# Optimization experiments

Measured on AMD Instinct MI355X. Metric: run time of the kernel, lower is better.

## Reference

```python
import jax, jax.numpy as jnp
import numpy as np
from jax import lax

BN_EPS = 1e-5
DELTA_FRAC = 0.7


def ternarize(t):
    """Per-row (dim 0) ternarization: delta = 0.7*mean|t_i|, alpha = mean of |t_i| above delta."""
    B = t.shape[0]
    flat = t.reshape(B, -1)                       # [B, n]
    absf = jnp.abs(flat)
    n = flat.shape[1]
    d = DELTA_FRAC * absf.sum(axis=1) / n         # [B]
    mask = absf > d[:, None]                      # strict >, matching torch code
    count = mask.sum(axis=1).astype(flat.dtype)
    alpha = (absf * mask).sum(axis=1) / count     # [B]
    tern = jnp.where(flat > d[:, None], 1.0, 0.0) + jnp.where(flat < -d[:, None], -1.0, 0.0)
    return (tern * alpha[:, None]).reshape(t.shape)


def conv2d(x, w, b):
    out = lax.conv_general_dilated(x, w, window_strides=(1, 1), padding='VALID',
                                   dimension_numbers=('NCHW', 'OIHW', 'NCHW'))
    return out + b[None, :, None, None]


def maxpool2(x):
    return lax.reduce_window(x, -jnp.inf, lax.max, (1, 1, 2, 2), (1, 1, 2, 2), 'VALID')


def batchnorm_eval(x, gamma, beta):
    # eval-mode BN with running_mean=0, running_var=1
    inv = 1.0 / np.sqrt(1.0 + BN_EPS)
    return x * (gamma[None, :, None, None] * inv) + beta[None, :, None, None]


def setup_inputs() -> dict:
    key = jax.random.key(0)
    ks = jax.random.split(key, 12)
    B = 2048
    inp = {
        'x': jax.random.normal(ks[0], (B, 1, 28, 28), dtype=jnp.float32),
        'conv1_w': jax.random.normal(ks[1], (32, 1, 5, 5), dtype=jnp.float32) * 0.1,
        'conv1_b': jax.random.normal(ks[2], (32,), dtype=jnp.float32) * 0.1,
        'bn1_g': jax.random.normal(ks[3], (32,), dtype=jnp.float32) * 0.1 + 1.0,
        'bn1_b': jax.random.normal(ks[4], (32,), dtype=jnp.float32) * 0.1,
        'conv2_w': jax.random.normal(ks[5], (64, 32, 5, 5), dtype=jnp.float32) * 0.05,
        'conv2_b': jax.random.normal(ks[6], (64,), dtype=jnp.float32) * 0.1,
        'bn2_g': jax.random.normal(ks[7], (64,), dtype=jnp.float32) * 0.1 + 1.0,
        'bn2_b': jax.random.normal(ks[8], (64,), dtype=jnp.float32) * 0.1,
        'fc1_w': jax.random.normal(ks[9], (512, 1024), dtype=jnp.float32) * 0.03,
        'fc1_b': jax.random.normal(ks[10], (512,), dtype=jnp.float32) * 0.1,
        'fc2_w': jax.random.normal(ks[11], (10, 512), dtype=jnp.float32) * 0.05,
        'fc2_b': jnp.zeros((10,), dtype=jnp.float32),
    }
    return inp


def reference(x, conv1_w, conv1_b, bn1_g, bn1_b, conv2_w, conv2_b, bn2_g, bn2_b,
              fc1_w, fc1_b, fc2_w, fc2_b):
    h = ternarize(conv2d(x, conv1_w, conv1_b))            # [B,32,24,24]
    h = jax.nn.relu(maxpool2(batchnorm_eval(h, bn1_g, bn1_b)))  # [B,32,12,12]
    h = ternarize(conv2d(h, conv2_w, conv2_b))            # [B,64,8,8]
    h = jax.nn.relu(maxpool2(batchnorm_eval(h, bn2_g, bn2_b)))  # [B,64,4,4]
    h = h.reshape(-1, 1024)
    h = jax.nn.relu(ternarize(h @ fc1_w.T + fc1_b))       # [B,512]
    out = ternarize(h @ fc2_w.T + fc2_b)                  # [B,10]
    return out
```

## Files before the change

kernel.cpp:

```cpp
#include <hip/hip_runtime.h>

#define BATCH 2048

__device__ __forceinline__ float blockReduceSumF(float v, float* red, int tid, int nwaves) {
  #pragma unroll
  for (int off = 32; off > 0; off >>= 1) v += __shfl_xor(v, off);
  __syncthreads();
  if ((tid & 63) == 0) red[tid >> 6] = v;
  __syncthreads();
  if (tid == 0) {
    float s = red[0];
    for (int i = 1; i < nwaves; i++) s += red[i];
    red[31] = s;
  }
  __syncthreads();
  return red[31];
}

__device__ __forceinline__ float2 blockReduceSum2F(float a, float b, float* red, int tid, int nwaves) {
  #pragma unroll
  for (int off = 32; off > 0; off >>= 1) { a += __shfl_xor(a, off); b += __shfl_xor(b, off); }
  __syncthreads();
  if ((tid & 63) == 0) { red[tid >> 6] = a; red[(tid >> 6) + 16] = b; }
  __syncthreads();
  if (tid == 0) {
    float sa = red[0], sb = red[16];
    for (int i = 1; i < nwaves; i++) { sa += red[i]; sb += red[16 + i]; }
    red[30] = sa; red[31] = sb;
  }
  __syncthreads();
  return make_float2(red[30], red[31]);
}

__device__ __forceinline__ float groupReduce4w(float v, float* seg, int tj) {
  #pragma unroll
  for (int off = 32; off > 0; off >>= 1) v += __shfl_xor(v, off);
  __syncthreads();
  if ((tj & 63) == 0) seg[tj >> 6] = v;
  __syncthreads();
  return (seg[0] + seg[1]) + (seg[2] + seg[3]);
}

__global__ void k0_w2t(const float* __restrict__ w2, float* __restrict__ w2t2) {
  int i = blockIdx.x * 256 + threadIdx.x;
  if (i >= 57344) return;
  int cc = i / 1792;
  int r = i - cc * 1792;
  int c2 = r / 28;
  int k = r - c2 * 28;
  w2t2[i] = (k < 25) ? w2[c2 * 800 + cc * 25 + k] : 0.0f;
}

__global__ __launch_bounds__(512, 4) void k1_conv1(
    const float* __restrict__ x, const float* __restrict__ w1, const float* __restrict__ b1,
    signed char* __restrict__ s1full, float* __restrict__ alpha1) {
  __shared__ float xs[784];
  __shared__ float wsm[800];
  __shared__ float red[32];

  const int tid = threadIdx.x;
  const int smp = blockIdx.x;

  for (int j = tid; j < 784; j += 512) xs[j] = x[smp * 784 + j];
  for (int j = tid; j < 800; j += 512) wsm[j] = w1[j];
  __syncthreads();

  const int c = tid >> 4;
  const int g = tid & 15;
  const float bias = b1[c];
  const float* wc = &wsm[c * 25];

  float a[36];
  float asum = 0.0f;
  #pragma unroll
  for (int tt = 0; tt < 3; tt++) {
    const int t = g + (tt << 4);
    const int r = t >> 1;
    const int hx = (t & 1) * 12;
    float acc[12];
    #pragma unroll
    for (int i = 0; i < 12; i++) acc[i] = bias;
    #pragma unroll
    for (int ky = 0; ky < 5; ky++) {
      const float* xp = &xs[(r + ky) * 28 + hx];
      float xrow[16];
      *(float4*)&xrow[0]  = *(const float4*)&xp[0];
      *(float4*)&xrow[4]  = *(const float4*)&xp[4];
      *(float4*)&xrow[8]  = *(const float4*)&xp[8];
      *(float4*)&xrow[12] = *(const float4*)&xp[12];
      #pragma unroll
      for (int kx = 0; kx < 5; kx++) {
        const float w = wc[ky * 5 + kx];
        #pragma unroll
        for (int i = 0; i < 12; i++) acc[i] = fmaf(xrow[i + kx], w, acc[i]);
      }
    }
    #pragma unroll
    for (int i = 0; i < 12; i++) { a[tt * 12 + i] = acc[i]; asum += fabsf(acc[i]); }
  }

  float tot = blockReduceSumF(asum, red, tid, 8);
  float delta = (0.7f * tot) / 18432.0f;

  float msum = 0.0f, mcnt = 0.0f;
  #pragma unroll
  for (int i = 0; i < 36; i++) {
    float fa = fabsf(a[i]);
    if (fa > delta) { msum += fa; mcnt += 1.0f; }
  }
  float2 mm = blockReduceSum2F(msum, mcnt, red, tid, 8);
  if (tid == 0) alpha1[smp] = (mm.y > 0.0f) ? (mm.x / mm.y) : 0.0f;

  signed char* sp = s1full + (size_t)smp * 18432 + c * 576 + g * 12;
  #pragma unroll
  for (int tt = 0; tt < 3; tt++) {
    int s_[12];
    #pragma unroll
    for (int i = 0; i < 12; i++) {
      float v = a[tt * 12 + i];
      s_[i] = (v > delta) ? 1 : ((v < -delta) ? -1 : 0);
    }
    unsigned u0 = (s_[0] & 0xFF) | ((s_[1] & 0xFF) << 8) | ((s_[2] & 0xFF) << 16) |
                  (((unsigned)(s_[3] & 0xFF)) << 24);
    unsigned u1 = (s_[4] & 0xFF) | ((s_[5] & 0xFF) << 8) | ((s_[6] & 0xFF) << 16) |
                  (((unsigned)(s_[7] & 0xFF)) << 24);
    unsigned u2 = (s_[8] & 0xFF) | ((s_[9] & 0xFF) << 8) | ((s_[10] & 0xFF) << 16) |
                  (((unsigned)(s_[11] & 0xFF)) << 24);
    unsigned* wq = (unsigned*)(sp + tt * 192);
    wq[0] = u0; wq[1] = u1; wq[2] = u2;
  }
}

__global__ __launch_bounds__(256, 3) void k2_conv2(
    const signed char* __restrict__ s1full, const float* __restrict__ alpha1,
    const float* __restrict__ w2t2, const float* __restrict__ b2,
    const float* __restrict__ g1, const float* __restrict__ bt1,
    signed char* __restrict__ s2full, float* __restrict__ alpha2) {
  __shared__ float pooled[4608];
  __shared__ float g1l[32], bt1l[32];
  __shared__ float red[32];

  const int tid = threadIdx.x;
  const int smp = blockIdx.x;
  const float BNINV = (float)(1.0 / sqrt(1.0 + 1e-5));

  if (tid < 32) { g1l[tid] = g1[tid] * BNINV; bt1l[tid] = bt1[tid]; }
  __syncthreads();

  const float a1 = alpha1[smp];
  {
    const int ci = tid >> 3;
    const int o8 = tid & 7;
    int r = o8 * 18;
    int py = (o8 * 3) >> 1;
    int px = r - py * 12;
    const signed char* sbase = s1full + (size_t)smp * 18432 + ci * 576;
    float* pout = &pooled[ci * 144];
    const float gg = g1l[ci], bb = bt1l[ci];
    #pragma unroll
    for (int k = 0; k < 18; k++) {
      const signed char* sp = sbase + py * 48 + px * 2;
      char2 t0 = *(const char2*)sp;
      char2 t1 = *(const char2*)(sp + 24);
      float m = -1e30f;
      { float v = ((float)t0.x * a1) * gg + bb; m = (v > m) ? v : m; }
      { float v = ((float)t0.y * a1) * gg + bb; m = (v > m) ? v : m; }
      { float v = ((float)t1.x * a1) * gg + bb; m = (v > m) ? v : m; }
      { float v = ((float)t1.y * a1) * gg + bb; m = (v > m) ? v : m; }
      pout[py * 12 + px] = (m > 0.0f) ? m : 0.0f;
      px++;
      if (px == 12) { px = 0; py++; }
    }
  }
  __syncthreads();

  const int c2 = tid >> 2;
  const int q = tid & 3;
  const int r0 = q << 1;
  const float bias = b2[c2];
  float acc0[8], acc1[8];
  #pragma unroll
  for (int i = 0; i < 8; i++) { acc0[i] = bias; acc1[i] = bias; }

  const float4* wp = ((const float4*)w2t2) + c2 * 7;
  const float* pb = &pooled[r0 * 12];
  #pragma unroll 1
  for (int cc = 0; cc < 32; cc++) {
    const float4 W0 = wp[0], W1 = wp[1], W2 = wp[2], W3 = wp[3],
                 W4 = wp[4], W5 = wp[5], W6 = wp[6];
    const float wk[25] = {W0.x, W0.y, W0.z, W0.w, W1.x, W1.y, W1.z, W1.w,
                          W2.x, W2.y, W2.z, W2.w, W3.x, W3.y, W3.z, W3.w,
                          W4.x, W4.y, W4.z, W4.w, W5.x, W5.y, W5.z, W5.w, W6.x};
    #pragma unroll
    for (int t = 0; t < 6; t++) {
      float row[12];
      *(float4*)&row[0] = *(const float4*)&pb[t * 12];
      *(float4*)&row[4] = *(const float4*)&pb[t * 12 + 4];
      *(float4*)&row[8] = *(const float4*)&pb[t * 12 + 8];
      #pragma unroll
      for (int ky = 0; ky < 5; ky++) {
        const int i = t - ky;
        if (i == 0) {
          #pragma unroll
          for (int kx = 0; kx < 5; kx++) {
            const float w = wk[ky * 5 + kx];
            #pragma unroll
            for (int ox = 0; ox < 8; ox++) acc0[ox] = fmaf(row[ox + kx], w, acc0[ox]);
          }
        } else if (i == 1) {
          #pragma unroll
          for (int kx = 0; kx < 5; kx++) {
            const float w = wk[ky * 5 + kx];
            #pragma unroll
            for (int ox = 0; ox < 8; ox++) acc1[ox] = fmaf(row[ox + kx], w, acc1[ox]);
          }
        }
      }
    }
    wp += 448;
    pb += 144;
  }

  float asum = 0.0f;
  #pragma unroll
  for (int i = 0; i < 8; i++) asum += fabsf(acc0[i]) + fabsf(acc1[i]);
  float tot = blockReduceSumF(asum, red, tid, 4);
  float delta = (0.7f * tot) / 4096.0f;

  float msum = 0.0f, mcnt = 0.0f;
  #pragma unroll
  for (int i = 0; i < 8; i++) {
    float f0 = fabsf(acc0[i]);
    if (f0 > delta) { msum += f0; mcnt += 1.0f; }
    float f1 = fabsf(acc1[i]);
    if (f1 > delta) { msum += f1; mcnt += 1.0f; }
  }
  float2 mm = blockReduceSum2F(msum, mcnt, red, tid, 4);
  if (tid == 0) alpha2[smp] = (mm.y > 0.0f) ? (mm.x / mm.y) : 0.0f;

  int t_[16];
  #pragma unroll
  for (int ox = 0; ox < 8; ox++) {
    float v = acc0[ox];
    t_[ox] = (v > delta) ? 1 : ((v < -delta) ? -1 : 0);
  }
  #pragma unroll
  for (int ox = 0; ox < 8; ox++) {
    float v = acc1[ox];
    t_[8 + ox] = (v > delta) ? 1 : ((v < -delta) ? -1 : 0);
  }
  unsigned u0 = (t_[0] & 0xFF) | ((t_[1] & 0xFF) << 8) | ((t_[2] & 0xFF) << 16) |
                (((unsigned)(t_[3] & 0xFF)) << 24);
  unsigned u1 = (t_[4] & 0xFF) | ((t_[5] & 0xFF) << 8) | ((t_[6] & 0xFF) << 16) |
                (((unsigned)(t_[7] & 0xFF)) << 24);
  unsigned u2 = (t_[8] & 0xFF) | ((t_[9] & 0xFF) << 8) | ((t_[10] & 0xFF) << 16) |
                (((unsigned)(t_[11] & 0xFF)) << 24);
  unsigned u3 = (t_[12] & 0xFF) | ((t_[13] & 0xFF) << 8) | ((t_[14] & 0xFF) << 16) |
                (((unsigned)(t_[15] & 0xFF)) << 24);
  *(uint4*)(s2full + (size_t)smp * 4096 + c2 * 64 + r0 * 8) = make_uint4(u0, u1, u2, u3);
}

__global__ void k0_transpose(const float* __restrict__ w1f, float* __restrict__ w1t) {
  int i = blockIdx.x * 256 + threadIdx.x;
  int k = i >> 9;
  int o = i & 511;
  w1t[i] = w1f[o * 1024 + k];
}

__global__ __launch_bounds__(1024, 4) void k3_fc(
    const signed char* __restrict__ s2full, const float* __restrict__ alpha2,
    const float* __restrict__ w1t, const float* __restrict__ f1b,
    const float* __restrict__ w2f, const float* __restrict__ f2b,
    const float* __restrict__ g2, const float* __restrict__ bt2,
    float* __restrict__ out) {
  __shared__ float S[16384];
  __shared__ float fco[4][512];
  __shared__ float g2l[64], bt2l[64];
  __shared__ float redm[4][4];
  __shared__ float out2[4][10];

  const int tid = threadIdx.x;
  const int blk = blockIdx.x;
  const float BNINV = (float)(1.0 / sqrt(1.0 + 1e-5));

  if (tid < 64) { g2l[tid] = g2[tid] * BNINV; bt2l[tid] = bt2[tid]; }
  __syncthreads();

  float* h4 = S;
  for (int e = tid; e < 4096; e += 1024) {
    int j = e >> 2;
    int s = e & 3;
    int cc = j >> 4;
    int r = j & 15;
    int py = r >> 2;
    int px = r & 3;
    const signed char* sp = s2full + (size_t)(blk * 4 + s) * 4096 + cc * 64 + (py * 2) * 8 + px * 2;
    float a2 = alpha2[blk * 4 + s];
    float m = -1e30f;
    #pragma unroll
    for (int dy = 0; dy < 2; dy++)
      #pragma unroll
      for (int dx = 0; dx < 2; dx++) {
        float v = ((float)sp[dy * 8 + dx] * a2) * g2l[cc] + bt2l[cc];
        m = (v > m) ? v : m;
      }
    h4[j * 4 + s] = (m > 0.0f) ? m : 0.0f;
  }
  __syncthreads();

  const int kp = tid >> 7;
  const int og = tid & 127;
  float a00=0,a01=0,a02=0,a03=0, a10=0,a11=0,a12=0,a13=0;
  float a20=0,a21=0,a22=0,a23=0, a30=0,a31=0,a32=0,a33=0;
  const float4* w4 = (const float4*)w1t;
  const float4* h44 = (const float4*)h4;
  const int kbase = kp << 7;
  for (int kk = 0; kk < 128; kk++) {
    const int k = kbase + kk;
    const float4 wv = w4[(k << 7) + og];
    const float4 hv = h44[k];
    a00 = fmaf(hv.x, wv.x, a00); a01 = fmaf(hv.y, wv.x, a01);
    a02 = fmaf(hv.z, wv.x, a02); a03 = fmaf(hv.w, wv.x, a03);
    a10 = fmaf(hv.x, wv.y, a10); a11 = fmaf(hv.y, wv.y, a11);
    a12 = fmaf(hv.z, wv.y, a12); a13 = fmaf(hv.w, wv.y, a13);
    a20 = fmaf(hv.x, wv.z, a20); a21 = fmaf(hv.y, wv.z, a21);
    a22 = fmaf(hv.z, wv.z, a22); a23 = fmaf(hv.w, wv.z, a23);
    a30 = fmaf(hv.x, wv.w, a30); a31 = fmaf(hv.y, wv.w, a31);
    a32 = fmaf(hv.z, wv.w, a32); a33 = fmaf(hv.w, wv.w, a33);
  }
  __syncthreads();
  {
    float4* p4 = (float4*)S;
    const int base = (kp << 9) + (og << 2);
    p4[base + 0] = make_float4(a00, a01, a02, a03);
    p4[base + 1] = make_float4(a10, a11, a12, a13);
    p4[base + 2] = make_float4(a20, a21, a22, a23);
    p4[base + 3] = make_float4(a30, a31, a32, a33);
  }
  __syncthreads();

  for (int p = tid; p < 2048; p += 1024) {
    int o = p >> 2;
    int s = p & 3;
    float v = S[p];
    #pragma unroll
    for (int kp2 = 1; kp2 < 8; kp2++) v += S[kp2 * 2048 + p];
    fco[s][o] = v + f1b[o];
  }
  __syncthreads();

  float (*h3)[512] = (float(*)[512])S;
  const int sg = tid >> 8;
  const int tj = tid & 255;
  float v0 = fco[sg][tj];
  float v1 = fco[sg][tj + 256];
  float av0 = fabsf(v0), av1 = fabsf(v1);
  float tot = groupReduce4w(av0 + av1, redm[sg], tj);
  float delta = (0.7f * tot) / 512.0f;
  float m0 = (av0 > delta) ? av0 : 0.0f;
  float m1 = (av1 > delta) ? av1 : 0.0f;
  float msum = groupReduce4w(m0 + m1, redm[sg], tj);
  float mcnt = groupReduce4w(((av0 > delta) ? 1.0f : 0.0f) + ((av1 > delta) ? 1.0f : 0.0f),
                             redm[sg], tj);
  float alpha3 = (mcnt > 0.0f) ? (msum / mcnt) : 0.0f;
  {
    float t0 = (v0 > delta) ? 1.0f : ((v0 < -delta) ? -1.0f : 0.0f);
    float hv0 = t0 * alpha3;
    h3[sg][tj] = (hv0 > 0.0f) ? hv0 : 0.0f;
    float t1 = (v1 > delta) ? 1.0f : ((v1 < -delta) ? -1.0f : 0.0f);
    float hv1 = t1 * alpha3;
    h3[sg][tj + 256] = (hv1 > 0.0f) ? hv1 : 0.0f;
  }
  __syncthreads();

  const int lane = tid & 63;
  const int wid = tid >> 6;
  for (int t = wid; t < 40; t += 16) {
    int s = t / 10;
    int o = t - s * 10;
    float acc = 0.0f;
    #pragma unroll
    for (int m = 0; m < 8; m++) {
      int j = lane + (m << 6);
      acc = fmaf(h3[s][j], w2f[o * 512 + j], acc);
    }
    #pragma unroll
    for (int off = 32; off > 0; off >>= 1) acc += __shfl_xor(acc, off);
    if (lane == 0) out2[s][o] = acc + f2b[o];
  }
  __syncthreads();

  if (tid < 4) {
    int s = tid;
    float t2 = 0.0f;
    for (int i = 0; i < 10; i++) t2 += fabsf(out2[s][i]);
    float d = (0.7f * t2) / 10.0f;
    float ms = 0.0f, mc = 0.0f;
    for (int i = 0; i < 10; i++) {
      float a = fabsf(out2[s][i]);
      if (a > d) { ms += a; mc += 1.0f; }
    }
    float al = (mc > 0.0f) ? (ms / mc) : 0.0f;
    for (int i = 0; i < 10; i++) {
      float vv = out2[s][i];
      float sv = (vv > d) ? 1.0f : ((vv < -d) ? -1.0f : 0.0f);
      out[(size_t)(blk * 4 + s) * 10 + i] = sv * al;
    }
  }
}

__global__ void k_marker(float* __restrict__ out, int n, float val) {
  int i = blockIdx.x * 256 + threadIdx.x;
  if (i < n) out[i] = val;
}

extern "C" void kernel_launch(void* const* d_in, const int* in_sizes, int n_in,
                              void* d_out, int out_size, void* d_ws, size_t ws_size,
                              hipStream_t stream) {
  float* out = (float*)d_out;

  static const int expect[13] = {1605632, 800, 32, 32, 32, 51200, 64, 64, 64,
                                 524288, 512, 5120, 10};
  float marker = 0.0f;
  if (n_in != 13) marker = 304.0f;
  else {
    for (int i = 0; i < 13; i++)
      if (in_sizes[i] != expect[i]) { marker = 320.0f + 16.0f * i; break; }
  }
  if (marker == 0.0f && out_size != 20480) marker = 560.0f;

  float* alpha1 = (float*)d_ws;
  float* alpha2 = alpha1 + BATCH;
  float* w2t2   = alpha2 + BATCH;
  signed char* s1full = (signed char*)(w2t2 + 57344);
  signed char* s2full = s1full + (size_t)BATCH * 18432;
  size_t needed = (size_t)((s2full + (size_t)BATCH * 4096) - (signed char*)d_ws);
  if (marker == 0.0f && ws_size < needed) marker = 576.0f;

  if (marker != 0.0f) {
    k_marker<<<dim3((out_size + 255) / 256), dim3(256), 0, stream>>>(out, out_size, marker);
    return;
  }

  const float* x   = (const float*)d_in[0];
  const float* c1w = (const float*)d_in[1];
  const float* c1b = (const float*)d_in[2];
  const float* g1  = (const float*)d_in[3];
  const float* bt1 = (const float*)d_in[4];
  const float* c2w = (const float*)d_in[5];
  const float* c2b = (const float*)d_in[6];
  const float* g2  = (const float*)d_in[7];
  const float* bt2 = (const float*)d_in[8];
  const float* f1w = (const float*)d_in[9];
  const float* f1b = (const float*)d_in[10];
  const float* f2w = (const float*)d_in[11];
  const float* f2b = (const float*)d_in[12];

  float* w1t = (float*)s1full;

  k0_w2t<<<dim3(224), dim3(256), 0, stream>>>(c2w, w2t2);
  k1_conv1<<<dim3(BATCH), dim3(512), 0, stream>>>(x, c1w, c1b, s1full, alpha1);
  k2_conv2<<<dim3(BATCH), dim3(256), 0, stream>>>(s1full, alpha1, w2t2, c2b, g1, bt1, s2full, alpha2);
  k0_transpose<<<dim3(2048), dim3(256), 0, stream>>>(f1w, w1t);
  k3_fc<<<dim3(BATCH / 4), dim3(1024), 0, stream>>>(s2full, alpha2, w1t, f1b, f2w, f2b, g2, bt2, out);
}
```

Baseline: 347.1 us.

## Compute full 8x8 conv2 output per thread with single-wave blocks

The conv2 kernel now uses one 64-thread wave per sample, and each thread computes a whole 8x8 output map for its output channel instead of two rows. Each loaded pooled row and weight set now feeds more FMAs, which cuts shared-memory and weight traffic per FMA. Because the block is a single wave, the block reductions become in-wave shuffle reductions and the __syncthreads-based LDS reductions go away. In exchange, each thread holds 64 accumulators, so register pressure rises, and fewer waves share each CU's LDS, which can weaken latency hiding in the pooling and accumulation phases.

```diff
diff --git a/kernel.cpp b/kernel.cpp
--- a/kernel.cpp
+++ b/kernel.cpp
@@ -39,6 +39,21 @@
   if ((tj & 63) == 0) seg[tj >> 6] = v;
   __syncthreads();
   return (seg[0] + seg[1]) + (seg[2] + seg[3]);
+}
+
+__device__ __forceinline__ float emulReduce256(float a0, float a1, float a2, float a3) {
+  #pragma unroll
+  for (int off = 8; off >= 1; off >>= 1) {
+    a0 += __shfl_xor(a0, off);
+    a1 += __shfl_xor(a1, off);
+    a2 += __shfl_xor(a2, off);
+    a3 += __shfl_xor(a3, off);
+  }
+  float b0 = a0 + a2;
+  float b1 = a1 + a3;
+  float w  = b0 + b1;
+  float r0 = __shfl(w, 0), r1 = __shfl(w, 16), r2 = __shfl(w, 32), r3 = __shfl(w, 48);
+  return ((r0 + r1) + r2) + r3;
 }
 
 __global__ void k0_w2t(const float* __restrict__ w2, float* __restrict__ w2t2) {
@@ -131,14 +146,13 @@
   }
 }
 
-__global__ __launch_bounds__(256, 3) void k2_conv2(
+__global__ __launch_bounds__(64, 2) void k2_conv2(
     const signed char* __restrict__ s1full, const float* __restrict__ alpha1,
     const float* __restrict__ w2t2, const float* __restrict__ b2,
     const float* __restrict__ g1, const float* __restrict__ bt1,
     signed char* __restrict__ s2full, float* __restrict__ alpha2) {
   __shared__ float pooled[4608];
   __shared__ float g1l[32], bt1l[32];
-  __shared__ float red[32];
 
   const int tid = threadIdx.x;
   const int smp = blockIdx.x;
@@ -149,41 +163,40 @@
 
   const float a1 = alpha1[smp];
   {
-    const int ci = tid >> 3;
-    const int o8 = tid & 7;
-    int r = o8 * 18;
-    int py = (o8 * 3) >> 1;
-    int px = r - py * 12;
+    const int ci = tid >> 1;
+    const int h  = tid & 1;
     const signed char* sbase = s1full + (size_t)smp * 18432 + ci * 576;
     float* pout = &pooled[ci * 144];
     const float gg = g1l[ci], bb = bt1l[ci];
     #pragma unroll
-    for (int k = 0; k < 18; k++) {
-      const signed char* sp = sbase + py * 48 + px * 2;
-      char2 t0 = *(const char2*)sp;
-      char2 t1 = *(const char2*)(sp + 24);
-      float m = -1e30f;
-      { float v = ((float)t0.x * a1) * gg + bb; m = (v > m) ? v : m; }
-      { float v = ((float)t0.y * a1) * gg + bb; m = (v > m) ? v : m; }
-      { float v = ((float)t1.x * a1) * gg + bb; m = (v > m) ? v : m; }
-      { float v = ((float)t1.y * a1) * gg + bb; m = (v > m) ? v : m; }
-      pout[py * 12 + px] = (m > 0.0f) ? m : 0.0f;
-      px++;
-      if (px == 12) { px = 0; py++; }
-    }
-  }
-  __syncthreads();
-
-  const int c2 = tid >> 2;
-  const int q = tid & 3;
-  const int r0 = q << 1;
+    for (int rr = 0; rr < 6; rr++) {
+      const int py = h * 6 + rr;
+      #pragma unroll
+      for (int px = 0; px < 12; px++) {
+        const signed char* sp = sbase + py * 48 + px * 2;
+        char2 t0 = *(const char2*)sp;
+        char2 t1 = *(const char2*)(sp + 24);
+        float m = -1e30f;
+        { float v = ((float)t0.x * a1) * gg + bb; m = (v > m) ? v : m; }
+        { float v = ((float)t0.y * a1) * gg + bb; m = (v > m) ? v : m; }
+        { float v = ((float)t1.x * a1) * gg + bb; m = (v > m) ? v : m; }
+        { float v = ((float)t1.y * a1) * gg + bb; m = (v > m) ? v : m; }
+        pout[py * 12 + px] = (m > 0.0f) ? m : 0.0f;
+      }
+    }
+  }
+  __syncthreads();
+
+  const int c2 = tid;
   const float bias = b2[c2];
-  float acc0[8], acc1[8];
-  #pragma unroll
-  for (int i = 0; i < 8; i++) { acc0[i] = bias; acc1[i] = bias; }
+  float acc[8][8];
+  #pragma unroll
+  for (int r = 0; r < 8; r++)
+    #pragma unroll
+    for (int i = 0; i < 8; i++) acc[r][i] = bias;
 
   const float4* wp = ((const float4*)w2t2) + c2 * 7;
-  const float* pb = &pooled[r0 * 12];
+  const float* pb = pooled;
   #pragma unroll 1
   for (int cc = 0; cc < 32; cc++) {
     const float4 W0 = wp[0], W1 = wp[1], W2 = wp[2], W3 = wp[3],
@@ -192,27 +205,20 @@
                           W2.x, W2.y, W2.z, W2.w, W3.x, W3.y, W3.z, W3.w,
                           W4.x, W4.y, W4.z, W4.w, W5.x, W5.y, W5.z, W5.w, W6.x};
     #pragma unroll
-    for (int t = 0; t < 6; t++) {
+    for (int t = 0; t < 12; t++) {
       float row[12];
       *(float4*)&row[0] = *(const float4*)&pb[t * 12];
       *(float4*)&row[4] = *(const float4*)&pb[t * 12 + 4];
       *(float4*)&row[8] = *(const float4*)&pb[t * 12 + 8];
       #pragma unroll
       for (int ky = 0; ky < 5; ky++) {
-        const int i = t - ky;
-        if (i == 0) {
+        const int r = t - ky;
+        if (r >= 0 && r < 8) {
           #pragma unroll
           for (int kx = 0; kx < 5; kx++) {
             const float w = wk[ky * 5 + kx];
             #pragma unroll
-            for (int ox = 0; ox < 8; ox++) acc0[ox] = fmaf(row[ox + kx], w, acc0[ox]);
-          }
-        } else if (i == 1) {
-          #pragma unroll
-          for (int kx = 0; kx < 5; kx++) {
-            const float w = wk[ky * 5 + kx];
-            #pragma unroll
-            for (int ox = 0; ox < 8; ox++) acc1[ox] = fmaf(row[ox + kx], w, acc1[ox]);
+            for (int i = 0; i < 8; i++) acc[r][i] = fmaf(row[i + kx], w, acc[r][i]);
           }
         }
       }
@@ -221,43 +227,62 @@
     pb += 144;
   }
 
-  float asum = 0.0f;
-  #pragma unroll
-  for (int i = 0; i < 8; i++) asum += fabsf(acc0[i]) + fabsf(acc1[i]);
-  float tot = blockReduceSumF(asum, red, tid, 4);
+  float as0, as1, as2, as3;
+  {
+    float s[4];
+    #pragma unroll
+    for (int qq = 0; qq < 4; qq++) {
+      float v = 0.0f;
+      #pragma unroll
+      for (int i = 0; i < 8; i++) v += fabsf(acc[2 * qq][i]) + fabsf(acc[2 * qq + 1][i]);
+      s[qq] = v;
+    }
+    as0 = s[0]; as1 = s[1]; as2 = s[2]; as3 = s[3];
+  }
+  float tot = emulReduce256(as0, as1, as2, as3);
   float delta = (0.7f * tot) / 4096.0f;
 
-  float msum = 0.0f, mcnt = 0.0f;
-  #pragma unroll
-  for (int i = 0; i < 8; i++) {
-    float f0 = fabsf(acc0[i]);
-    if (f0 > delta) { msum += f0; mcnt += 1.0f; }
-    float f1 = fabsf(acc1[i]);
-    if (f1 > delta) { msum += f1; mcnt += 1.0f; }
-  }
-  float2 mm = blockReduceSum2F(msum, mcnt, red, tid, 4);
-  if (tid == 0) alpha2[smp] = (mm.y > 0.0f) ? (mm.x / mm.y) : 0.0f;
-
-  int t_[16];
-  #pragma unroll
-  for (int ox = 0; ox < 8; ox++) {
-    float v = acc0[ox];
-    t_[ox] = (v > delta) ? 1 : ((v < -delta) ? -1 : 0);
-  }
-  #pragma unroll
-  for (int ox = 0; ox < 8; ox++) {
-    float v = acc1[ox];
-    t_[8 + ox] = (v > delta) ? 1 : ((v < -delta) ? -1 : 0);
-  }
-  unsigned u0 = (t_[0] & 0xFF) | ((t_[1] & 0xFF) << 8) | ((t_[2] & 0xFF) << 16) |
-                (((unsigned)(t_[3] & 0xFF)) << 24);
-  unsigned u1 = (t_[4] & 0xFF) | ((t_[5] & 0xFF) << 8) | ((t_[6] & 0xFF) << 16) |
-                (((unsigned)(t_[7] & 0xFF)) << 24);
-  unsigned u2 = (t_[8] & 0xFF) | ((t_[9] & 0xFF) << 8) | ((t_[10] & 0xFF) << 16) |
-                (((unsigned)(t_[11] & 0xFF)) << 24);
-  unsigned u3 = (t_[12] & 0xFF) | ((t_[13] & 0xFF) << 8) | ((t_[14] & 0xFF) << 16) |
-                (((unsigned)(t_[15] & 0xFF)) << 24);
-  *(uint4*)(s2full + (size_t)smp * 4096 + c2 * 64 + r0 * 8) = make_uint4(u0, u1, u2, u3);
+  float ms[4], mc[4];
+  #pragma unroll
+  for (int qq = 0; qq < 4; qq++) {
+    float msum = 0.0f, mcnt = 0.0f;
+    #pragma unroll
+    for (int i = 0; i < 8; i++) {
+      float f0 = fabsf(acc[2 * qq][i]);
+      if (f0 > delta) { msum += f0; mcnt += 1.0f; }
+      float f1 = fabsf(acc[2 * qq + 1][i]);
+      if (f1 > delta) { msum += f1; mcnt += 1.0f; }
+    }
+    ms[qq] = msum; mc[qq] = mcnt;
+  }
+  float msumT = emulReduce256(ms[0], ms[1], ms[2], ms[3]);
+  float mcntT = emulReduce256(mc[0], mc[1], mc[2], mc[3]);
+  if (tid == 0) alpha2[smp] = (mcntT > 0.0f) ? (msumT / mcntT) : 0.0f;
+
+  signed char* so = s2full + (size_t)smp * 4096 + c2 * 64;
+  #pragma unroll
+  for (int pr = 0; pr < 4; pr++) {
+    int t_[16];
+    #pragma unroll
+    for (int i = 0; i < 8; i++) {
+      float v = acc[2 * pr][i];
+      t_[i] = (v > delta) ? 1 : ((v < -delta) ? -1 : 0);
+    }
+    #pragma unroll
+    for (int i = 0; i < 8; i++) {
+      float v = acc[2 * pr + 1][i];
+      t_[8 + i] = (v > delta) ? 1 : ((v < -delta) ? -1 : 0);
+    }
+    unsigned u0 = (t_[0] & 0xFF) | ((t_[1] & 0xFF) << 8) | ((t_[2] & 0xFF) << 16) |
+                  (((unsigned)(t_[3] & 0xFF)) << 24);
+    unsigned u1 = (t_[4] & 0xFF) | ((t_[5] & 0xFF) << 8) | ((t_[6] & 0xFF) << 16) |
+                  (((unsigned)(t_[7] & 0xFF)) << 24);
+    unsigned u2 = (t_[8] & 0xFF) | ((t_[9] & 0xFF) << 8) | ((t_[10] & 0xFF) << 16) |
+                  (((unsigned)(t_[11] & 0xFF)) << 24);
+    unsigned u3 = (t_[12] & 0xFF) | ((t_[13] & 0xFF) << 8) | ((t_[14] & 0xFF) << 16) |
+                  (((unsigned)(t_[15] & 0xFF)) << 24);
+    *(uint4*)(so + pr * 16) = make_uint4(u0, u1, u2, u3);
+  }
 }
 
 __global__ void k0_transpose(const float* __restrict__ w1f, float* __restrict__ w1t) {
@@ -460,7 +485,7 @@
 
   k0_w2t<<<dim3(224), dim3(256), 0, stream>>>(c2w, w2t2);
   k1_conv1<<<dim3(BATCH), dim3(512), 0, stream>>>(x, c1w, c1b, s1full, alpha1);
-  k2_conv2<<<dim3(BATCH), dim3(256), 0, stream>>>(s1full, alpha1, w2t2, c2b, g1, bt1, s2full, alpha2);
+  k2_conv2<<<dim3(BATCH), dim3(64), 0, stream>>>(s1full, alpha1, w2t2, c2b, g1, bt1, s2full, alpha2);
   k0_transpose<<<dim3(2048), dim3(256), 0, stream>>>(f1w, w1t);
   k3_fc<<<dim3(BATCH / 4), dim3(1024), 0, stream>>>(s2full, alpha2, w1t, f1b, f2w, f2b, g2, bt2, out);
 }
```

Measured after the change: 320.8 us. 1.08x faster.

## Halve conv2 block size and compute four output rows per thread

Applied to the files above, without the earlier changes.

The conv2 kernel now runs 128 threads per sample instead of 256, and each thread accumulates a 4x8 output tile instead of 2x8. Each loaded pooled input row is now reused across up to four output rows, and each weight fetch is amortised over twice as many outputs, which cuts LDS and global weight traffic per FMA. The reductions are rewritten into a helper that emulates the previous summation grouping, and the pooling prologue is turned into a strided loop. The larger accumulator set raises register pressure and gives fewer threads per sample, which may lower occupancy or latency hiding.

```diff
diff --git a/kernel.cpp b/kernel.cpp
--- a/kernel.cpp
+++ b/kernel.cpp
@@ -39,6 +39,18 @@
   if ((tj & 63) == 0) seg[tj >> 6] = v;
   __syncthreads();
   return (seg[0] + seg[1]) + (seg[2] + seg[3]);
+}
+
+__device__ __forceinline__ float emulR128(float a0, float a1, float* red, int tid) {
+  #pragma unroll
+  for (int off = 16; off >= 2; off >>= 1) { a0 += __shfl_xor(a0, off); a1 += __shfl_xor(a1, off); }
+  a0 += __shfl_xor(a0, 1);
+  a1 += __shfl_xor(a1, 1);
+  float w = a0 + a1;
+  __syncthreads();
+  if ((tid & 31) == 0) red[tid >> 5] = w;
+  __syncthreads();
+  return ((red[0] + red[1]) + red[2]) + red[3];
 }
 
 __global__ void k0_w2t(const float* __restrict__ w2, float* __restrict__ w2t2) {
@@ -131,7 +143,7 @@
   }
 }
 
-__global__ __launch_bounds__(256, 3) void k2_conv2(
+__global__ __launch_bounds__(128, 4) void k2_conv2(
     const signed char* __restrict__ s1full, const float* __restrict__ alpha1,
     const float* __restrict__ w2t2, const float* __restrict__ b2,
     const float* __restrict__ g1, const float* __restrict__ bt1,
@@ -148,42 +160,34 @@
   __syncthreads();
 
   const float a1 = alpha1[smp];
-  {
-    const int ci = tid >> 3;
-    const int o8 = tid & 7;
-    int r = o8 * 18;
-    int py = (o8 * 3) >> 1;
+  for (int j = tid; j < 4608; j += 128) {
+    int ci = j / 144;
+    int r = j - ci * 144;
+    int py = r / 12;
     int px = r - py * 12;
-    const signed char* sbase = s1full + (size_t)smp * 18432 + ci * 576;
-    float* pout = &pooled[ci * 144];
-    const float gg = g1l[ci], bb = bt1l[ci];
-    #pragma unroll
-    for (int k = 0; k < 18; k++) {
-      const signed char* sp = sbase + py * 48 + px * 2;
-      char2 t0 = *(const char2*)sp;
-      char2 t1 = *(const char2*)(sp + 24);
-      float m = -1e30f;
-      { float v = ((float)t0.x * a1) * gg + bb; m = (v > m) ? v : m; }
-      { float v = ((float)t0.y * a1) * gg + bb; m = (v > m) ? v : m; }
-      { float v = ((float)t1.x * a1) * gg + bb; m = (v > m) ? v : m; }
-      { float v = ((float)t1.y * a1) * gg + bb; m = (v > m) ? v : m; }
-      pout[py * 12 + px] = (m > 0.0f) ? m : 0.0f;
-      px++;
-      if (px == 12) { px = 0; py++; }
-    }
-  }
-  __syncthreads();
-
-  const int c2 = tid >> 2;
-  const int q = tid & 3;
-  const int r0 = q << 1;
+    const signed char* sp = s1full + (size_t)smp * 18432 + ci * 576 + py * 48 + px * 2;
+    char2 t0 = *(const char2*)sp;
+    char2 t1 = *(const char2*)(sp + 24);
+    float m = -1e30f;
+    { float v = ((float)t0.x * a1) * g1l[ci] + bt1l[ci]; m = (v > m) ? v : m; }
+    { float v = ((float)t0.y * a1) * g1l[ci] + bt1l[ci]; m = (v > m) ? v : m; }
+    { float v = ((float)t1.x * a1) * g1l[ci] + bt1l[ci]; m = (v > m) ? v : m; }
+    { float v = ((float)t1.y * a1) * g1l[ci] + bt1l[ci]; m = (v > m) ? v : m; }
+    pooled[j] = (m > 0.0f) ? m : 0.0f;
+  }
+  __syncthreads();
+
+  const int c2 = tid >> 1;
+  const int h = tid & 1;
   const float bias = b2[c2];
-  float acc0[8], acc1[8];
-  #pragma unroll
-  for (int i = 0; i < 8; i++) { acc0[i] = bias; acc1[i] = bias; }
+  float acc[4][8];
+  #pragma unroll
+  for (int r = 0; r < 4; r++)
+    #pragma unroll
+    for (int i = 0; i < 8; i++) acc[r][i] = bias;
 
   const float4* wp = ((const float4*)w2t2) + c2 * 7;
-  const float* pb = &pooled[r0 * 12];
+  const float* pb = pooled + h * 48;
   #pragma unroll 1
   for (int cc = 0; cc < 32; cc++) {
     const float4 W0 = wp[0], W1 = wp[1], W2 = wp[2], W3 = wp[3],
@@ -192,27 +196,20 @@
                           W2.x, W2.y, W2.z, W2.w, W3.x, W3.y, W3.z, W3.w,
                           W4.x, W4.y, W4.z, W4.w, W5.x, W5.y, W5.z, W5.w, W6.x};
     #pragma unroll
-    for (int t = 0; t < 6; t++) {
+    for (int tt = 0; tt < 8; tt++) {
       float row[12];
-      *(float4*)&row[0] = *(const float4*)&pb[t * 12];
-      *(float4*)&row[4] = *(const float4*)&pb[t * 12 + 4];
-      *(float4*)&row[8] = *(const float4*)&pb[t * 12 + 8];
+      *(float4*)&row[0] = *(const float4*)&pb[tt * 12];
+      *(float4*)&row[4] = *(const float4*)&pb[tt * 12 + 4];
+      *(float4*)&row[8] = *(const float4*)&pb[tt * 12 + 8];
       #pragma unroll
       for (int ky = 0; ky < 5; ky++) {
-        const int i = t - ky;
-        if (i == 0) {
+        const int lr = tt - ky;
+        if (lr >= 0 && lr < 4) {
           #pragma unroll
           for (int kx = 0; kx < 5; kx++) {
             const float w = wk[ky * 5 + kx];
             #pragma unroll
-            for (int ox = 0; ox < 8; ox++) acc0[ox] = fmaf(row[ox + kx], w, acc0[ox]);
-          }
-        } else if (i == 1) {
-          #pragma unroll
-          for (int kx = 0; kx < 5; kx++) {
-            const float w = wk[ky * 5 + kx];
-            #pragma unroll
-            for (int ox = 0; ox < 8; ox++) acc1[ox] = fmaf(row[ox + kx], w, acc1[ox]);
+            for (int i = 0; i < 8; i++) acc[lr][i] = fmaf(row[i + kx], w, acc[lr][i]);
           }
         }
       }
@@ -221,43 +218,57 @@
     pb += 144;
   }
 
-  float asum = 0.0f;
-  #pragma unroll
-  for (int i = 0; i < 8; i++) asum += fabsf(acc0[i]) + fabsf(acc1[i]);
-  float tot = blockReduceSumF(asum, red, tid, 4);
+  float as0 = 0.0f, as1 = 0.0f;
+  #pragma unroll
+  for (int i = 0; i < 8; i++) as0 += fabsf(acc[0][i]) + fabsf(acc[1][i]);
+  #pragma unroll
+  for (int i = 0; i < 8; i++) as1 += fabsf(acc[2][i]) + fabsf(acc[3][i]);
+  float tot = emulR128(as0, as1, red, tid);
   float delta = (0.7f * tot) / 4096.0f;
 
-  float msum = 0.0f, mcnt = 0.0f;
+  float ms0 = 0.0f, mc0 = 0.0f, ms1 = 0.0f, mc1 = 0.0f;
   #pragma unroll
   for (int i = 0; i < 8; i++) {
-    float f0 = fabsf(acc0[i]);
-    if (f0 > delta) { msum += f0; mcnt += 1.0f; }
-    float f1 = fabsf(acc1[i]);
-    if (f1 > delta) { msum += f1; mcnt += 1.0f; }
-  }
-  float2 mm = blockReduceSum2F(msum, mcnt, red, tid, 4);
-  if (tid == 0) alpha2[smp] = (mm.y > 0.0f) ? (mm.x / mm.y) : 0.0f;
-
-  int t_[16];
-  #pragma unroll
-  for (int ox = 0; ox < 8; ox++) {
-    float v = acc0[ox];
-    t_[ox] = (v > delta) ? 1 : ((v < -delta) ? -1 : 0);
-  }
-  #pragma unroll
-  for (int ox = 0; ox < 8; ox++) {
-    float v = acc1[ox];
-    t_[8 + ox] = (v > delta) ? 1 : ((v < -delta) ? -1 : 0);
-  }
-  unsigned u0 = (t_[0] & 0xFF) | ((t_[1] & 0xFF) << 8) | ((t_[2] & 0xFF) << 16) |
-                (((unsigned)(t_[3] & 0xFF)) << 24);
-  unsigned u1 = (t_[4] & 0xFF) | ((t_[5] & 0xFF) << 8) | ((t_[6] & 0xFF) << 16) |
-                (((unsigned)(t_[7] & 0xFF)) << 24);
-  unsigned u2 = (t_[8] & 0xFF) | ((t_[9] & 0xFF) << 8) | ((t_[10] & 0xFF) << 16) |
-                (((unsigned)(t_[11] & 0xFF)) << 24);
-  unsigned u3 = (t_[12] & 0xFF) | ((t_[13] & 0xFF) << 8) | ((t_[14] & 0xFF) << 16) |
-                (((unsigned)(t_[15] & 0xFF)) << 24);
-  *(uint4*)(s2full + (size_t)smp * 4096 + c2 * 64 + r0 * 8) = make_uint4(u0, u1, u2, u3);
+    float f0 = fabsf(acc[0][i]);
+    if (f0 > delta) { ms0 += f0; mc0 += 1.0f; }
+    float f1 = fabsf(acc[1][i]);
+    if (f1 > delta) { ms0 += f1; mc0 += 1.0f; }
+  }
+  #pragma unroll
+  for (int i = 0; i < 8; i++) {
+    float f0 = fabsf(acc[2][i]);
+    if (f0 > delta) { ms1 += f0; mc1 += 1.0f; }
+    float f1 = fabsf(acc[3][i]);
+    if (f1 > delta) { ms1 += f1; mc1 += 1.0f; }
+  }
+  float msumT = emulR128(ms0, ms1, red, tid);
+  float mcntT = emulR128(mc0, mc1, red, tid);
+  if (tid == 0) alpha2[smp] = (mcntT > 0.0f) ? (msumT / mcntT) : 0.0f;
+
+  signed char* so = s2full + (size_t)smp * 4096 + c2 * 64 + h * 32;
+  #pragma unroll
+  for (int pr = 0; pr < 2; pr++) {
+    int t_[16];
+    #pragma unroll
+    for (int i = 0; i < 8; i++) {
+      float v = acc[2 * pr][i];
+      t_[i] = (v > delta) ? 1 : ((v < -delta) ? -1 : 0);
+    }
+    #pragma unroll
+    for (int i = 0; i < 8; i++) {
+      float v = acc[2 * pr + 1][i];
+      t_[8 + i] = (v > delta) ? 1 : ((v < -delta) ? -1 : 0);
+    }
+    unsigned u0 = (t_[0] & 0xFF) | ((t_[1] & 0xFF) << 8) | ((t_[2] & 0xFF) << 16) |
+                  (((unsigned)(t_[3] & 0xFF)) << 24);
+    unsigned u1 = (t_[4] & 0xFF) | ((t_[5] & 0xFF) << 8) | ((t_[6] & 0xFF) << 16) |
+                  (((unsigned)(t_[7] & 0xFF)) << 24);
+    unsigned u2 = (t_[8] & 0xFF) | ((t_[9] & 0xFF) << 8) | ((t_[10] & 0xFF) << 16) |
+                  (((unsigned)(t_[11] & 0xFF)) << 24);
+    unsigned u3 = (t_[12] & 0xFF) | ((t_[13] & 0xFF) << 8) | ((t_[14] & 0xFF) << 16) |
+                  (((unsigned)(t_[15] & 0xFF)) << 24);
+    *(uint4*)(so + pr * 16) = make_uint4(u0, u1, u2, u3);
+  }
 }
 
 __global__ void k0_transpose(const float* __restrict__ w1f, float* __restrict__ w1t) {
@@ -460,7 +471,7 @@
 
   k0_w2t<<<dim3(224), dim3(256), 0, stream>>>(c2w, w2t2);
   k1_conv1<<<dim3(BATCH), dim3(512), 0, stream>>>(x, c1w, c1b, s1full, alpha1);
-  k2_conv2<<<dim3(BATCH), dim3(256), 0, stream>>>(s1full, alpha1, w2t2, c2b, g1, bt1, s2full, alpha2);
+  k2_conv2<<<dim3(BATCH), dim3(128), 0, stream>>>(s1full, alpha1, w2t2, c2b, g1, bt1, s2full, alpha2);
   k0_transpose<<<dim3(2048), dim3(256), 0, stream>>>(f1w, w1t);
   k3_fc<<<dim3(BATCH / 4), dim3(1024), 0, stream>>>(s2full, alpha2, w1t, f1b, f2w, f2b, g2, bt2, out);
 }
```

Measured after the change: 332.3 us. -4.3%, faster.
